# Kernel tuning notes

Measured on AMD Instinct MI355X. Metric: run time of the kernel, lower is better.

The kernel has to match this reference:

```python
import jax, jax.numpy as jnp
import numpy as np

T, D, H, E, K = 8192, 2048, 1408, 8, 2


def setup_inputs() -> dict:
    key = jax.random.key(0)
    ks = jax.random.split(key, 6)
    x = jax.random.normal(ks[0], (T, D), dtype=jnp.float32)
    topK_indices = jax.random.randint(ks[1], (T, K), 0, E, dtype=jnp.int64)
    raw = jax.random.uniform(ks[2], (T, K), dtype=jnp.float32)
    topK_scores = raw / jnp.sum(raw, axis=1, keepdims=True)  # softmax-like normalized gate scores
    scale = 0.02
    W_gate = jax.random.normal(ks[3], (E, D, H), dtype=jnp.float32) * scale
    W_up = jax.random.normal(ks[4], (E, D, H), dtype=jnp.float32) * scale
    W_down = jax.random.normal(ks[5], (E, H, D), dtype=jnp.float32) * scale
    return {"x": x, "topK_indices": topK_indices, "topK_scores": topK_scores,
            "W_gate": W_gate, "W_up": W_up, "W_down": W_down}


def reference(x, topK_indices, topK_scores, W_gate, W_up, W_down):
    # Faithful math: y[t] = sum_s score[t,s] * Expert_{idx[t,s]}(x[t])
    # Regrouped by expert (same as torch sort/gather/scatter-add version):
    # combine[t,e] = sum_s score[t,s] * [idx[t,s]==e]; y = sum_e combine[:,e,None]*FFN_e(x)
    num_experts = W_gate.shape[0]
    one_hot = jax.nn.one_hot(topK_indices, num_experts, dtype=x.dtype)  # [T,K,E]
    combine = jnp.einsum("tke,tk->te", one_hot, topK_scores)  # [T,E]
    # SwiGLU expert FFN (LinearGLUExperts): down(silu(gate(x)) * up(x))
    h = jax.nn.silu(jnp.einsum("td,edh->eth", x, W_gate)) * jnp.einsum("td,edh->eth", x, W_up)
    # weight expert outputs by gate scores and scatter-combine (einsum fuses the index_add)
    y = jnp.einsum("te,eth,ehd->td", combine, h, W_down)
    return y
```

## Files before the change

### kernel.cpp

```cpp
#include <hip/hip_runtime.h>
#include <hip/hip_bf16.h>

#define TT 8192
#define DD 2048
#define HH 1408
#define EE 8
#define KTOP 2
#define NA (TT * KTOP)

typedef __attribute__((ext_vector_type(8))) short bh8;
typedef __attribute__((ext_vector_type(4))) float f4;

typedef __attribute__((address_space(1))) const void gconst_t;
typedef __attribute__((address_space(3))) void lds_t;

__device__ __forceinline__ void glds16(const void* g, void* l) {
  __builtin_amdgcn_global_load_lds((gconst_t*)g, (lds_t*)l, 16, 0, 0);
}

__device__ __forceinline__ float silu_f(float x) { return x / (1.f + __expf(-x)); }

__device__ __forceinline__ unsigned short bf16_bits(float x) {
  __hip_bfloat16 h = __float2bfloat16(x);
  return *reinterpret_cast<unsigned short*>(&h);
}

__global__ __launch_bounds__(1024) void k_book(const int* __restrict__ idx,
                                               const float* __restrict__ sc,
                                               int* __restrict__ off,
                                               int* __restrict__ rows_token,
                                               float* __restrict__ rows_score,
                                               int* __restrict__ pos) {
  __shared__ int cnt[EE];
  __shared__ int cur[EE];
  __shared__ int offs[EE + 1];
  const int tid = threadIdx.x;
  if (tid < EE) cnt[tid] = 0;
  __syncthreads();
#pragma unroll
  for (int j = 0; j < NA / 1024; ++j)
    atomicAdd(&cnt[idx[tid + j * 1024]], 1);
  __syncthreads();
  if (tid == 0) {
    int a = 0;
    for (int e = 0; e < EE; ++e) { offs[e] = a; cur[e] = a; a += cnt[e]; }
    offs[EE] = a;
  }
  __syncthreads();
  if (tid <= EE) off[tid] = offs[tid];
#pragma unroll
  for (int j = 0; j < NA / 1024; ++j) {
    int i = tid + j * 1024;
    int e = idx[i];
    int p = atomicAdd(&cur[e], 1);
    rows_token[p] = i >> 1;
    rows_score[p] = sc[i];
    pos[i] = p;
  }
}

__global__ __launch_bounds__(512) void k_prep(
    const float* __restrict__ x, __hip_bfloat16* __restrict__ xb,
    const float* __restrict__ Wg, const float* __restrict__ Wu,
    const float* __restrict__ Wd, __hip_bfloat16* __restrict__ Wgb,
    __hip_bfloat16* __restrict__ Wub, __hip_bfloat16* __restrict__ Wdb) {
  const int bid = blockIdx.x;
  const int tid = threadIdx.x;
  if (bid < 2048) {
    const float4* s4 = reinterpret_cast<const float4*>(x);
#pragma unroll
    for (int j = 0; j < 4; ++j) {
      int i = bid * 2048 + j * 512 + tid;
      float4 v = s4[i];
      union { ushort4 u; __hip_bfloat16 h[4]; } o;
      o.h[0] = __float2bfloat16(v.x); o.h[1] = __float2bfloat16(v.y);
      o.h[2] = __float2bfloat16(v.z); o.h[3] = __float2bfloat16(v.w);
      reinterpret_cast<ushort4*>(xb)[i] = o.u;
    }
    return;
  }
  __shared__ float t[128][129];
  const float* s;
  __hip_bfloat16* d;
  int R, C, rt, ct;
  if (bid < 4864) {
    int tno = bid - 2048;
    ct = tno % 11; tno /= 11;
    rt = tno % 16; tno /= 16;
    int e = tno & 7, sel = tno >> 3;
    R = DD; C = HH;
    s = (sel ? Wu : Wg) + (size_t)e * DD * HH;
    d = (sel ? Wub : Wgb) + (size_t)e * DD * HH;
  } else {
    int tno = bid - 4864;
    ct = tno % 16; tno /= 16;
    rt = tno % 11; tno /= 11;
    int e = tno;
    R = HH; C = DD;
    s = Wd + (size_t)e * DD * HH;
    d = Wdb + (size_t)e * DD * HH;
  }
  const int c0 = ct * 128, r0 = rt * 128;
#pragma unroll
  for (int j = 0; j < 8; ++j) {
    int f = tid + 512 * j;
    int row = f >> 5, c4 = (f & 31) << 2;
    float4 v = *reinterpret_cast<const float4*>(&s[(size_t)(r0 + row) * C + c0 + c4]);
    t[row][c4] = v.x; t[row][c4 + 1] = v.y; t[row][c4 + 2] = v.z; t[row][c4 + 3] = v.w;
  }
  __syncthreads();
  const int l = tid & 63;
  const int wv = tid >> 6;
#pragma unroll
  for (int pp = 0; pp < 16; ++pp) {
    int j = wv + (pp << 3);
    unsigned lo = bf16_bits(t[2 * l][j]);
    unsigned hi = bf16_bits(t[2 * l + 1][j]);
    unsigned* dp = reinterpret_cast<unsigned*>(d + (size_t)(c0 + j) * R + r0);
    dp[l] = lo | (hi << 16);
  }
}

__global__ void k_combine(const __hip_bfloat16* __restrict__ ybuf,
                          const int* __restrict__ pos, float* __restrict__ y) {
  int i = blockIdx.x * 256 + threadIdx.x;
  int t = i >> 8;
  int d0 = (i & 255) << 3;
  const uint4 a = *reinterpret_cast<const uint4*>(ybuf + (size_t)pos[2 * t] * DD + d0);
  const uint4 b = *reinterpret_cast<const uint4*>(ybuf + (size_t)pos[2 * t + 1] * DD + d0);
  float* o = y + (size_t)t * DD + d0;
  unsigned au[4] = {a.x, a.y, a.z, a.w}, bu[4] = {b.x, b.y, b.z, b.w};
  float r[8];
#pragma unroll
  for (int j = 0; j < 4; ++j) {
    r[2 * j] = __uint_as_float(au[j] << 16) + __uint_as_float(bu[j] << 16);
    r[2 * j + 1] = __uint_as_float(au[j] & 0xffff0000u) + __uint_as_float(bu[j] & 0xffff0000u);
  }
  reinterpret_cast<float4*>(o)[0] = (float4){r[0], r[1], r[2], r[3]};
  reinterpret_cast<float4*>(o)[1] = (float4){r[4], r[5], r[6], r[7]};
}

__global__ __launch_bounds__(256, 2) void k_gemm1(
    const __hip_bfloat16* __restrict__ xb,
    const __hip_bfloat16* __restrict__ Wgb,
    const __hip_bfloat16* __restrict__ Wub,
    const int* __restrict__ rows_token,
    const int* __restrict__ off,
    __hip_bfloat16* __restrict__ hbuf,
    int e0) {
  const int e = blockIdx.z + e0;
  const int oe = off[e];
  const int ne = off[e + 1] - oe;
  if (ne <= 0) return;
  const int n0 = blockIdx.x * 64;
  const int tid = threadIdx.x;
  const int lane = tid & 63;
  const int w = tid >> 6;

  __shared__ __hip_bfloat16 As[128 * 64];
  __shared__ __hip_bfloat16 Bs[128 * 64];

  const int kel = (((lane & 7) ^ (lane >> 3)) << 3);

  const __hip_bfloat16* bsrc[4];
#pragma unroll
  for (int i = 0; i < 4; ++i) {
    int bn = ((w * 4 + i) << 3) + (lane >> 3);
    const __hip_bfloat16* base =
        (bn < 64) ? (Wgb + ((size_t)e * HH + (n0 + bn)) * DD)
                  : (Wub + ((size_t)e * HH + (n0 + bn - 64)) * DD);
    bsrc[i] = base + kel;
  }

  for (int m0 = blockIdx.y * 128; m0 < ne; m0 += gridDim.y * 128) {
    const __hip_bfloat16* asrc[4];
#pragma unroll
    for (int i = 0; i < 4; ++i) {
      int r = ((w * 4 + i) << 3) + (lane >> 3);
      int rr = m0 + r; rr = rr < ne ? rr : ne - 1;
      asrc[i] = xb + (size_t)rows_token[oe + rr] * DD + kel;
    }

    f4 acc[2][8];
#pragma unroll
    for (int mf = 0; mf < 2; ++mf)
#pragma unroll
      for (int nf = 0; nf < 8; ++nf)
        acc[mf][nf] = (f4){0.f, 0.f, 0.f, 0.f};

    for (int k0 = 0; k0 < DD; k0 += 64) {
#pragma unroll
      for (int i = 0; i < 4; ++i) {
        glds16(asrc[i] + k0, As + ((w * 4 + i) << 9));
        glds16(bsrc[i] + k0, Bs + ((w * 4 + i) << 9));
      }
      __syncthreads();
#pragma unroll
      for (int kk = 0; kk < 2; ++kk) {
        const int kByte = (kk * 32 + ((lane >> 4) << 3)) * 2;
        bh8 a[2], b[8];
#pragma unroll
        for (int mf = 0; mf < 2; ++mf) {
          int row = (w << 5) + mf * 16 + (lane & 15);
          int ad = row * 128 + (kByte ^ ((row & 7) << 4));
          a[mf] = *reinterpret_cast<const bh8*>(reinterpret_cast<const char*>(As) + ad);
        }
#pragma unroll
        for (int nf = 0; nf < 8; ++nf) {
          int bn = nf * 16 + (lane & 15);
          int ad = bn * 128 + (kByte ^ ((bn & 7) << 4));
          b[nf] = *reinterpret_cast<const bh8*>(reinterpret_cast<const char*>(Bs) + ad);
        }
#pragma unroll
        for (int mf = 0; mf < 2; ++mf)
#pragma unroll
          for (int nf = 0; nf < 8; ++nf)
            acc[mf][nf] = __builtin_amdgcn_mfma_f32_16x16x32_bf16(a[mf], b[nf], acc[mf][nf], 0, 0, 0);
      }
      __syncthreads();
    }

    const int cb = n0 + (lane & 15);
#pragma unroll
    for (int mf = 0; mf < 2; ++mf) {
#pragma unroll
      for (int reg = 0; reg < 4; ++reg) {
        int grow = m0 + (w << 5) + mf * 16 + ((lane >> 4) << 2) + reg;
        if (grow < ne) {
          size_t hb = (size_t)(oe + grow) * HH;
#pragma unroll
          for (int nf = 0; nf < 4; ++nf) {
            float g = acc[mf][nf][reg];
            float u = acc[mf][nf + 4][reg];
            hbuf[hb + cb + nf * 16] = __float2bfloat16(silu_f(g) * u);
          }
        }
      }
    }
  }
}

__global__ __launch_bounds__(256, 2) void k_gemm2(
    const __hip_bfloat16* __restrict__ hbuf,
    const __hip_bfloat16* __restrict__ Wdb,
    const float* __restrict__ rows_score,
    const int* __restrict__ off,
    __hip_bfloat16* __restrict__ ybuf) {
  const int e = blockIdx.z;
  const int oe = off[e];
  const int ne = off[e + 1] - oe;
  if (ne <= 0) return;
  const int n0 = blockIdx.x * 128;
  const int tid = threadIdx.x;
  const int lane = tid & 63;
  const int w = tid >> 6;

  __shared__ __hip_bfloat16 As[128 * 64];
  __shared__ __hip_bfloat16 Bs[128 * 64];
  const int kel = (((lane & 7) ^ (lane >> 3)) << 3);

  const __hip_bfloat16* bsrc[4];
#pragma unroll
  for (int i = 0; i < 4; ++i) {
    int bn = ((w * 4 + i) << 3) + (lane >> 3);
    bsrc[i] = Wdb + ((size_t)e * DD + (n0 + bn)) * HH + kel;
  }

  for (int m0 = blockIdx.y * 128; m0 < ne; m0 += gridDim.y * 128) {
    const __hip_bfloat16* asrc[4];
#pragma unroll
    for (int i = 0; i < 4; ++i) {
      int r = ((w * 4 + i) << 3) + (lane >> 3);
      int rr = m0 + r; rr = rr < ne ? rr : ne - 1;
      asrc[i] = hbuf + (size_t)(oe + rr) * HH + kel;
    }

    f4 acc[2][8];
#pragma unroll
    for (int mf = 0; mf < 2; ++mf)
#pragma unroll
      for (int nf = 0; nf < 8; ++nf)
        acc[mf][nf] = (f4){0.f, 0.f, 0.f, 0.f};

    for (int k0 = 0; k0 < HH; k0 += 64) {
#pragma unroll
      for (int i = 0; i < 4; ++i) {
        glds16(asrc[i] + k0, As + ((w * 4 + i) << 9));
        glds16(bsrc[i] + k0, Bs + ((w * 4 + i) << 9));
      }
      __syncthreads();
#pragma unroll
      for (int kk = 0; kk < 2; ++kk) {
        const int kByte = (kk * 32 + ((lane >> 4) << 3)) * 2;
        bh8 a[2], b[8];
#pragma unroll
        for (int mf = 0; mf < 2; ++mf) {
          int row = (w << 5) + mf * 16 + (lane & 15);
          int ad = row * 128 + (kByte ^ ((row & 7) << 4));
          a[mf] = *reinterpret_cast<const bh8*>(reinterpret_cast<const char*>(As) + ad);
        }
#pragma unroll
        for (int nf = 0; nf < 8; ++nf) {
          int bn = nf * 16 + (lane & 15);
          int ad = bn * 128 + (kByte ^ ((bn & 7) << 4));
          b[nf] = *reinterpret_cast<const bh8*>(reinterpret_cast<const char*>(Bs) + ad);
        }
#pragma unroll
        for (int mf = 0; mf < 2; ++mf)
#pragma unroll
          for (int nf = 0; nf < 8; ++nf)
            acc[mf][nf] = __builtin_amdgcn_mfma_f32_16x16x32_bf16(a[mf], b[nf], acc[mf][nf], 0, 0, 0);
      }
      __syncthreads();
    }

#pragma unroll
    for (int mf = 0; mf < 2; ++mf) {
#pragma unroll
      for (int reg = 0; reg < 4; ++reg) {
        int grow = m0 + (w << 5) + mf * 16 + ((lane >> 4) << 2) + reg;
        if (grow < ne) {
          float sc = rows_score[oe + grow];
          __hip_bfloat16* yr = ybuf + (size_t)(oe + grow) * DD + n0 + (lane & 15);
#pragma unroll
          for (int nf = 0; nf < 8; ++nf)
            yr[nf * 16] = __float2bfloat16(sc * acc[mf][nf][reg]);
        }
      }
    }
  }
}

extern "C" void kernel_launch(void* const* d_in, const int* in_sizes, int n_in,
                              void* d_out, int out_size, void* d_ws, size_t ws_size,
                              hipStream_t stream) {
  const float* x = (const float*)d_in[0];
  const int* topk_idx = (const int*)d_in[1];
  const float* topk_sc = (const float*)d_in[2];
  const float* Wg = (const float*)d_in[3];
  const float* Wu = (const float*)d_in[4];
  const float* Wd = (const float*)d_in[5];
  float* y = (float*)d_out;

  char* p = (char*)d_ws;
  auto take = [&](size_t b) { char* r = p; p += (b + 255) & ~(size_t)255; return r; };
  int* off = (int*)take((EE + 1) * 4);
  int* rows_token = (int*)take((size_t)NA * 4);
  float* rows_score = (float*)take((size_t)NA * 4);
  int* pos = (int*)take((size_t)NA * 4);
  __hip_bfloat16* xb = (__hip_bfloat16*)take((size_t)TT * DD * 2);
  __hip_bfloat16* Wgb = (__hip_bfloat16*)take((size_t)EE * DD * HH * 2);
  __hip_bfloat16* Wub = (__hip_bfloat16*)take((size_t)EE * DD * HH * 2);
  __hip_bfloat16* Wdb = (__hip_bfloat16*)take((size_t)EE * DD * HH * 2);
  __hip_bfloat16* hbuf = (__hip_bfloat16*)take((size_t)NA * HH * 2);
  __hip_bfloat16* ybuf = (__hip_bfloat16*)take((size_t)NA * DD * 2);

  k_book<<<1, 1024, 0, stream>>>(topk_idx, topk_sc, off, rows_token, rows_score, pos);
  k_prep<<<6272, 512, 0, stream>>>(x, xb, Wg, Wu, Wd, Wgb, Wub, Wdb);
  k_gemm1<<<dim3(HH / 64, 17, 4), 256, 0, stream>>>(xb, Wgb, Wub, rows_token, off,
                                                    hbuf, 0);
  k_gemm1<<<dim3(HH / 64, 17, 4), 256, 0, stream>>>(xb, Wgb, Wub, rows_token, off,
                                                    hbuf, 4);
  k_gemm2<<<dim3(DD / 128, 17, EE), 256, 0, stream>>>(hbuf, Wdb, rows_score, off, ybuf);
  k_combine<<<TT * (DD / 8) / 256, 256, 0, stream>>>(ybuf, pos, y);
}
```

Measured before the change: 468.1 us.

## Use 2x2 wave tiling in MoE GEMMs, merge gemm1 launches, shrink prep tiles

Both expert GEMMs move from a 4x1 wave layout (each wave 32 rows x 128 cols) to a 2x2 layout (64x64 per wave). This cuts the LDS fragment loads per MFMA from 10 per 16 MFMAs to 8 per 16. In gemm1 the B tile now interleaves gate and up columns in 16-wide groups, so each wave holds matching gate/up accumulators for the SiLU epilogue. The two per-half-expert gemm1 launches become one launch over all experts. The weight transpose/convert prep kernel switches to 256 threads with 64-row tiles and a half-size LDS buffer, which gives more, smaller blocks.

Result: no change. 469.1 us (+0.2%).

```diff
diff --git a/kernel.cpp b/kernel.cpp
--- a/kernel.cpp
+++ b/kernel.cpp
@@ -20,9 +20,9 @@
 
 __device__ __forceinline__ float silu_f(float x) { return x / (1.f + __expf(-x)); }
 
-__device__ __forceinline__ unsigned short bf16_bits(float x) {
+__device__ __forceinline__ unsigned bf16_bits(float x) {
   __hip_bfloat16 h = __float2bfloat16(x);
-  return *reinterpret_cast<unsigned short*>(&h);
+  return (unsigned)*reinterpret_cast<unsigned short*>(&h);
 }
 
 __global__ __launch_bounds__(1024) void k_book(const int* __restrict__ idx,
@@ -59,18 +59,18 @@
   }
 }
 
-__global__ __launch_bounds__(512) void k_prep(
+__global__ __launch_bounds__(256) void k_prep(
     const float* __restrict__ x, __hip_bfloat16* __restrict__ xb,
     const float* __restrict__ Wg, const float* __restrict__ Wu,
     const float* __restrict__ Wd, __hip_bfloat16* __restrict__ Wgb,
     __hip_bfloat16* __restrict__ Wub, __hip_bfloat16* __restrict__ Wdb) {
   const int bid = blockIdx.x;
   const int tid = threadIdx.x;
-  if (bid < 2048) {
+  if (bid < 1024) {
     const float4* s4 = reinterpret_cast<const float4*>(x);
 #pragma unroll
-    for (int j = 0; j < 4; ++j) {
-      int i = bid * 2048 + j * 512 + tid;
+    for (int j = 0; j < 16; ++j) {
+      int i = bid * 4096 + j * 256 + tid;
       float4 v = s4[i];
       union { ushort4 u; __hip_bfloat16 h[4]; } o;
       o.h[0] = __float2bfloat16(v.x); o.h[1] = __float2bfloat16(v.y);
@@ -79,41 +79,40 @@
     }
     return;
   }
-  __shared__ float t[128][129];
+  __shared__ float t[64][129];
   const float* s;
   __hip_bfloat16* d;
   int R, C, rt, ct;
-  if (bid < 4864) {
-    int tno = bid - 2048;
+  if (bid < 6656) {
+    int tno = bid - 1024;
     ct = tno % 11; tno /= 11;
-    rt = tno % 16; tno /= 16;
+    rt = tno % 32; tno /= 32;
     int e = tno & 7, sel = tno >> 3;
     R = DD; C = HH;
     s = (sel ? Wu : Wg) + (size_t)e * DD * HH;
     d = (sel ? Wub : Wgb) + (size_t)e * DD * HH;
   } else {
-    int tno = bid - 4864;
+    int tno = bid - 6656;
     ct = tno % 16; tno /= 16;
-    rt = tno % 11; tno /= 11;
+    rt = tno % 22; tno /= 22;
     int e = tno;
     R = HH; C = DD;
     s = Wd + (size_t)e * DD * HH;
     d = Wdb + (size_t)e * DD * HH;
   }
-  const int c0 = ct * 128, r0 = rt * 128;
+  const int c0 = ct * 128, r0 = rt * 64;
 #pragma unroll
   for (int j = 0; j < 8; ++j) {
-    int f = tid + 512 * j;
+    int f = tid + 256 * j;
     int row = f >> 5, c4 = (f & 31) << 2;
     float4 v = *reinterpret_cast<const float4*>(&s[(size_t)(r0 + row) * C + c0 + c4]);
     t[row][c4] = v.x; t[row][c4 + 1] = v.y; t[row][c4 + 2] = v.z; t[row][c4 + 3] = v.w;
   }
   __syncthreads();
-  const int l = tid & 63;
-  const int wv = tid >> 6;
 #pragma unroll
   for (int pp = 0; pp < 16; ++pp) {
-    int j = wv + (pp << 3);
+    int g = pp * 256 + tid;
+    int j = g >> 5, l = g & 31;
     unsigned lo = bf16_bits(t[2 * l][j]);
     unsigned hi = bf16_bits(t[2 * l + 1][j]);
     unsigned* dp = reinterpret_cast<unsigned*>(d + (size_t)(c0 + j) * R + r0);
@@ -146,9 +145,8 @@
     const __hip_bfloat16* __restrict__ Wub,
     const int* __restrict__ rows_token,
     const int* __restrict__ off,
-    __hip_bfloat16* __restrict__ hbuf,
-    int e0) {
-  const int e = blockIdx.z + e0;
+    __hip_bfloat16* __restrict__ hbuf) {
+  const int e = blockIdx.z;
   const int oe = off[e];
   const int ne = off[e + 1] - oe;
   if (ne <= 0) return;
@@ -156,6 +154,9 @@
   const int tid = threadIdx.x;
   const int lane = tid & 63;
   const int w = tid >> 6;
+  const int wm = w >> 1, wn = w & 1;
+  const int l15 = lane & 15;
+  const int l4 = lane >> 4;
 
   __shared__ __hip_bfloat16 As[128 * 64];
   __shared__ __hip_bfloat16 Bs[128 * 64];
@@ -166,10 +167,9 @@
 #pragma unroll
   for (int i = 0; i < 4; ++i) {
     int bn = ((w * 4 + i) << 3) + (lane >> 3);
-    const __hip_bfloat16* base =
-        (bn < 64) ? (Wgb + ((size_t)e * HH + (n0 + bn)) * DD)
-                  : (Wub + ((size_t)e * HH + (n0 + bn - 64)) * DD);
-    bsrc[i] = base + kel;
+    int ts = (bn >> 4) & 1;
+    int hc = n0 + ((bn >> 5) << 4) + (bn & 15);
+    bsrc[i] = (ts ? Wub : Wgb) + ((size_t)e * HH + hc) * DD + kel;
   }
 
   for (int m0 = blockIdx.y * 128; m0 < ne; m0 += gridDim.y * 128) {
@@ -181,11 +181,11 @@
       asrc[i] = xb + (size_t)rows_token[oe + rr] * DD + kel;
     }
 
-    f4 acc[2][8];
-#pragma unroll
-    for (int mf = 0; mf < 2; ++mf)
-#pragma unroll
-      for (int nf = 0; nf < 8; ++nf)
+    f4 acc[4][4];
+#pragma unroll
+    for (int mf = 0; mf < 4; ++mf)
+#pragma unroll
+      for (int nf = 0; nf < 4; ++nf)
         acc[mf][nf] = (f4){0.f, 0.f, 0.f, 0.f};
 
     for (int k0 = 0; k0 < DD; k0 += 64) {
@@ -197,42 +197,41 @@
       __syncthreads();
 #pragma unroll
       for (int kk = 0; kk < 2; ++kk) {
-        const int kByte = (kk * 32 + ((lane >> 4) << 3)) * 2;
-        bh8 a[2], b[8];
-#pragma unroll
-        for (int mf = 0; mf < 2; ++mf) {
-          int row = (w << 5) + mf * 16 + (lane & 15);
+        const int kByte = (kk * 32 + (l4 << 3)) * 2;
+        bh8 a[4], b[4];
+#pragma unroll
+        for (int i = 0; i < 4; ++i) {
+          int row = (wm << 6) + (i << 4) + l15;
           int ad = row * 128 + (kByte ^ ((row & 7) << 4));
-          a[mf] = *reinterpret_cast<const bh8*>(reinterpret_cast<const char*>(As) + ad);
-        }
-#pragma unroll
-        for (int nf = 0; nf < 8; ++nf) {
-          int bn = nf * 16 + (lane & 15);
+          a[i] = *reinterpret_cast<const bh8*>(reinterpret_cast<const char*>(As) + ad);
+        }
+#pragma unroll
+        for (int i = 0; i < 4; ++i) {
+          int bn = (wn << 6) + (i << 4) + l15;
           int ad = bn * 128 + (kByte ^ ((bn & 7) << 4));
-          b[nf] = *reinterpret_cast<const bh8*>(reinterpret_cast<const char*>(Bs) + ad);
-        }
-#pragma unroll
-        for (int mf = 0; mf < 2; ++mf)
-#pragma unroll
-          for (int nf = 0; nf < 8; ++nf)
+          b[i] = *reinterpret_cast<const bh8*>(reinterpret_cast<const char*>(Bs) + ad);
+        }
+#pragma unroll
+        for (int mf = 0; mf < 4; ++mf)
+#pragma unroll
+          for (int nf = 0; nf < 4; ++nf)
             acc[mf][nf] = __builtin_amdgcn_mfma_f32_16x16x32_bf16(a[mf], b[nf], acc[mf][nf], 0, 0, 0);
       }
       __syncthreads();
     }
 
-    const int cb = n0 + (lane & 15);
-#pragma unroll
-    for (int mf = 0; mf < 2; ++mf) {
+#pragma unroll
+    for (int mf = 0; mf < 4; ++mf) {
 #pragma unroll
       for (int reg = 0; reg < 4; ++reg) {
-        int grow = m0 + (w << 5) + mf * 16 + ((lane >> 4) << 2) + reg;
+        int grow = m0 + (wm << 6) + (mf << 4) + (l4 << 2) + reg;
         if (grow < ne) {
           size_t hb = (size_t)(oe + grow) * HH;
 #pragma unroll
-          for (int nf = 0; nf < 4; ++nf) {
-            float g = acc[mf][nf][reg];
-            float u = acc[mf][nf + 4][reg];
-            hbuf[hb + cb + nf * 16] = __float2bfloat16(silu_f(g) * u);
+          for (int jn = 0; jn < 2; ++jn) {
+            float g = acc[mf][2 * jn][reg];
+            float u = acc[mf][2 * jn + 1][reg];
+            hbuf[hb + n0 + 32 * wn + 16 * jn + l15] = __float2bfloat16(silu_f(g) * u);
           }
         }
       }
@@ -254,6 +253,9 @@
   const int tid = threadIdx.x;
   const int lane = tid & 63;
   const int w = tid >> 6;
+  const int wm = w >> 1, wn = w & 1;
+  const int l15 = lane & 15;
+  const int l4 = lane >> 4;
 
   __shared__ __hip_bfloat16 As[128 * 64];
   __shared__ __hip_bfloat16 Bs[128 * 64];
@@ -275,11 +277,11 @@
       asrc[i] = hbuf + (size_t)(oe + rr) * HH + kel;
     }
 
-    f4 acc[2][8];
-#pragma unroll
-    for (int mf = 0; mf < 2; ++mf)
-#pragma unroll
-      for (int nf = 0; nf < 8; ++nf)
+    f4 acc[4][4];
+#pragma unroll
+    for (int mf = 0; mf < 4; ++mf)
+#pragma unroll
+      for (int nf = 0; nf < 4; ++nf)
         acc[mf][nf] = (f4){0.f, 0.f, 0.f, 0.f};
 
     for (int k0 = 0; k0 < HH; k0 += 64) {
@@ -291,39 +293,39 @@
       __syncthreads();
 #pragma unroll
       for (int kk = 0; kk < 2; ++kk) {
-        const int kByte = (kk * 32 + ((lane >> 4) << 3)) * 2;
-        bh8 a[2], b[8];
-#pragma unroll
-        for (int mf = 0; mf < 2; ++mf) {
-          int row = (w << 5) + mf * 16 + (lane & 15);
+        const int kByte = (kk * 32 + (l4 << 3)) * 2;
+        bh8 a[4], b[4];
+#pragma unroll
+        for (int i = 0; i < 4; ++i) {
+          int row = (wm << 6) + (i << 4) + l15;
           int ad = row * 128 + (kByte ^ ((row & 7) << 4));
-          a[mf] = *reinterpret_cast<const bh8*>(reinterpret_cast<const char*>(As) + ad);
-        }
-#pragma unroll
-        for (int nf = 0; nf < 8; ++nf) {
-          int bn = nf * 16 + (lane & 15);
+          a[i] = *reinterpret_cast<const bh8*>(reinterpret_cast<const char*>(As) + ad);
+        }
+#pragma unroll
+        for (int i = 0; i < 4; ++i) {
+          int bn = (wn << 6) + (i << 4) + l15;
           int ad = bn * 128 + (kByte ^ ((bn & 7) << 4));
-          b[nf] = *reinterpret_cast<const bh8*>(reinterpret_cast<const char*>(Bs) + ad);
-        }
-#pragma unroll
-        for (int mf = 0; mf < 2; ++mf)
-#pragma unroll
-          for (int nf = 0; nf < 8; ++nf)
+          b[i] = *reinterpret_cast<const bh8*>(reinterpret_cast<const char*>(Bs) + ad);
+        }
+#pragma unroll
+        for (int mf = 0; mf < 4; ++mf)
+#pragma unroll
+          for (int nf = 0; nf < 4; ++nf)
             acc[mf][nf] = __builtin_amdgcn_mfma_f32_16x16x32_bf16(a[mf], b[nf], acc[mf][nf], 0, 0, 0);
       }
       __syncthreads();
     }
 
 #pragma unroll
-    for (int mf = 0; mf < 2; ++mf) {
+    for (int mf = 0; mf < 4; ++mf) {
 #pragma unroll
       for (int reg = 0; reg < 4; ++reg) {
-        int grow = m0 + (w << 5) + mf * 16 + ((lane >> 4) << 2) + reg;
+        int grow = m0 + (wm << 6) + (mf << 4) + (l4 << 2) + reg;
         if (grow < ne) {
           float sc = rows_score[oe + grow];
-          __hip_bfloat16* yr = ybuf + (size_t)(oe + grow) * DD + n0 + (lane & 15);
-#pragma unroll
-          for (int nf = 0; nf < 8; ++nf)
+          __hip_bfloat16* yr = ybuf + (size_t)(oe + grow) * DD + n0 + (wn << 6) + l15;
+#pragma unroll
+          for (int nf = 0; nf < 4; ++nf)
             yr[nf * 16] = __float2bfloat16(sc * acc[mf][nf][reg]);
         }
       }
@@ -356,11 +358,8 @@
   __hip_bfloat16* ybuf = (__hip_bfloat16*)take((size_t)NA * DD * 2);
 
   k_book<<<1, 1024, 0, stream>>>(topk_idx, topk_sc, off, rows_token, rows_score, pos);
-  k_prep<<<6272, 512, 0, stream>>>(x, xb, Wg, Wu, Wd, Wgb, Wub, Wdb);
-  k_gemm1<<<dim3(HH / 64, 17, 4), 256, 0, stream>>>(xb, Wgb, Wub, rows_token, off,
-                                                    hbuf, 0);
-  k_gemm1<<<dim3(HH / 64, 17, 4), 256, 0, stream>>>(xb, Wgb, Wub, rows_token, off,
-                                                    hbuf, 4);
+  k_prep<<<9472, 256, 0, stream>>>(x, xb, Wg, Wu, Wd, Wgb, Wub, Wdb);
+  k_gemm1<<<dim3(HH / 64, 17, EE), 256, 0, stream>>>(xb, Wgb, Wub, rows_token, off, hbuf);
   k_gemm2<<<dim3(DD / 128, 17, EE), 256, 0, stream>>>(hbuf, Wdb, rows_score, off, ybuf);
   k_combine<<<TT * (DD / 8) / 256, 256, 0, stream>>>(ybuf, pos, y);
 }
```
